# Kernel tuning notes

Hardware: AMD Instinct MI355X
Metric: run time of the kernel (lower is better)

Reference implementation:

```python
import jax, jax.numpy as jnp
import numpy as np

SPATIAL_SHAPES = [(116, 200), (58, 100), (29, 50), (15, 25)]  # (H, W) per level
NUM_HEADS = 8
NUM_LEVELS = 4
NUM_POINTS = 8
NUM_Z = 4  # num_Z_anchors; NUM_POINTS must be divisible by NUM_Z
EMBED = 256


def _msda3d_forward(query, value, reference_points, w_off, b_off, w_attn, b_attn, w_val, b_val):
    bs, nq, _ = query.shape
    d = EMBED // NUM_HEADS
    # value projection -> (bs, num_value, heads, d)
    v = (value @ w_val + b_val).reshape(bs, -1, NUM_HEADS, d)
    # sampling offsets and attention weights from query
    off = (query @ w_off + b_off).reshape(bs, nq, NUM_HEADS, NUM_LEVELS, NUM_POINTS, 2)
    attn = (query @ w_attn + b_attn).reshape(bs, nq, NUM_HEADS, NUM_LEVELS * NUM_POINTS)
    attn = jax.nn.softmax(attn, axis=-1).reshape(bs, nq, NUM_HEADS, NUM_LEVELS, NUM_POINTS)
    # normalize offsets by (W, H) per level
    shapes = jnp.asarray(SPATIAL_SHAPES, dtype=query.dtype)  # (L,2) = (h,w)
    norm = jnp.stack([shapes[:, 1], shapes[:, 0]], axis=-1)  # (L,2) = (w,h)
    off = off / norm[None, None, None, :, None, :]
    # reference_points (bs,nq,Z,2) broadcast against offsets split over Z anchors
    p_per_z = NUM_POINTS // NUM_Z
    off = off.reshape(bs, nq, NUM_HEADS, NUM_LEVELS, p_per_z, NUM_Z, 2)
    loc = reference_points[:, :, None, None, None, :, :] + off
    loc = loc.reshape(bs, nq, NUM_HEADS, NUM_LEVELS, NUM_POINTS, 2)
    # per-level bilinear sampling (grid_sample, align_corners=False, zeros padding)
    out = jnp.zeros((bs, nq, NUM_HEADS, d), dtype=query.dtype)
    start = 0
    for lvl, (H, W) in enumerate(SPATIAL_SHAPES):
        v_l = v[:, start:start + H * W]  # (bs, H*W, heads, d)
        start += H * W
        locs = loc[:, :, :, lvl]  # (bs, nq, heads, P, 2) in [0,1]
        # grid = 2*loc-1, then unnormalize with align_corners=False: x = loc*W - 0.5
        x = locs[..., 0] * W - 0.5
        y = locs[..., 1] * H - 0.5
        x0 = jnp.floor(x)
        y0 = jnp.floor(y)
        lx = x - x0
        ly = y - y0
        x0i = x0.astype(jnp.int32)
        y0i = y0.astype(jnp.int32)
        samp = jnp.zeros((bs, nq, NUM_HEADS, NUM_POINTS, d), dtype=query.dtype)
        corners = ((0, 0, (1 - ly) * (1 - lx)), (0, 1, (1 - ly) * lx),
                   (1, 0, ly * (1 - lx)), (1, 1, ly * lx))
        for dy, dx, w in corners:
            xi = x0i + dx
            yi = y0i + dy
            valid = (xi >= 0) & (xi < W) & (yi >= 0) & (yi < H)
            idx = jnp.clip(yi, 0, H - 1) * W + jnp.clip(xi, 0, W - 1)  # (bs,nq,heads,P)
            # gather along flattened HW per (batch, head)
            idx2 = idx.transpose(0, 1, 3, 2).reshape(bs, nq * NUM_POINTS, NUM_HEADS)
            g = jnp.take_along_axis(v_l, idx2[..., None], axis=1)  # (bs, nq*P, heads, d)
            g = g.reshape(bs, nq, NUM_POINTS, NUM_HEADS, d).transpose(0, 1, 3, 2, 4)
            samp = samp + g * (w * valid.astype(query.dtype))[..., None]
        out = out + (samp * attn[:, :, :, lvl, :, None]).sum(axis=3)
    return out.reshape(bs, nq, EMBED)


def setup_inputs() -> dict:
    key = jax.random.key(0)
    ks = jax.random.split(key, 9)
    bs, nq = 6, 10000
    num_value = sum(h * w for h, w in SPATIAL_SHAPES)  # 30825
    return {
        "query": jax.random.normal(ks[0], (bs, nq, EMBED), jnp.float32),
        "value": jax.random.normal(ks[1], (bs, num_value, EMBED), jnp.float32),
        "reference_points": jax.random.uniform(ks[2], (bs, nq, NUM_Z, 2), jnp.float32),
        "w_off": jax.random.normal(ks[3], (EMBED, NUM_HEADS * NUM_LEVELS * NUM_POINTS * 2), jnp.float32) * 0.01,
        "b_off": jax.random.normal(ks[4], (NUM_HEADS * NUM_LEVELS * NUM_POINTS * 2,), jnp.float32) * 0.02,
        "w_attn": jax.random.normal(ks[5], (EMBED, NUM_HEADS * NUM_LEVELS * NUM_POINTS), jnp.float32) * 0.02,
        "b_attn": jnp.zeros((NUM_HEADS * NUM_LEVELS * NUM_POINTS,), jnp.float32),
        "w_val": jax.random.normal(ks[6], (EMBED, EMBED), jnp.float32) * 0.02,
        "b_val": jnp.zeros((EMBED,), jnp.float32),
    }


def reference(query, value, reference_points, w_off, b_off, w_attn, b_attn, w_val, b_val):
    return _msda3d_forward(query, value, reference_points, w_off, b_off, w_attn, b_attn, w_val, b_val)
```

## Files before the change

kernel.cpp:

```cpp
#include <hip/hip_runtime.h>
#include <hip/hip_bf16.h>

#define NQ 10000
#define BS 6
#define NV 30825

typedef __attribute__((ext_vector_type(8))) short bf16x8;
typedef __attribute__((ext_vector_type(8))) unsigned short u16x8;
typedef __attribute__((ext_vector_type(4))) float f32x4;
typedef __attribute__((ext_vector_type(2))) float f32x2;

__device__ __forceinline__ void gload_lds16(const void* g, void* l) {
  __builtin_amdgcn_global_load_lds(
      (const __attribute__((address_space(1))) unsigned int*)g,
      (__attribute__((address_space(3))) unsigned int*)l, 16, 0, 0);
}

__device__ __forceinline__ unsigned short bf_bits(float f) {
  __hip_bfloat16 h = __float2bfloat16(f);
  return *(unsigned short*)&h;
}

__global__ __launch_bounds__(256) void prep_weights_kernel(
    const float* __restrict__ w_val, const float* __restrict__ w_off,
    const float* __restrict__ w_attn, const float* __restrict__ b_off,
    const float* __restrict__ b_attn, unsigned short* __restrict__ wvalT,
    unsigned short* __restrict__ wpackT, float* __restrict__ bpack) {
  int i = blockIdx.x * 256 + threadIdx.x;
  if (i < 65536) {
    int n = i >> 8, k = i & 255;
    wvalT[i] = bf_bits(w_val[k * 256 + n]);
  } else if (i < 65536 + 196608) {
    int j = i - 65536;
    int n = j >> 8, k = j & 255;
    float v = (n < 512) ? w_off[k * 512 + n] : w_attn[k * 256 + (n - 512)];
    wpackT[j] = bf_bits(v);
  } else if (i < 65536 + 196608 + 768) {
    int j = i - 262144;
    bpack[j] = (j < 512) ? b_off[j] : b_attn[j - 512];
  }
}

__global__ __launch_bounds__(256) void gemm_mfma_kernel(
    const float* __restrict__ A, const unsigned short* __restrict__ WT,
    const float* __restrict__ bias, unsigned short* __restrict__ C, int M, int N) {
  __shared__ short As[128 * 64];
  __shared__ short Bs[128 * 64];
  const int tid = threadIdx.x;
  const int wv = tid >> 6;
  const int lane = tid & 63;
  const int wr = wv >> 1, wc = wv & 1;
  const int m0 = blockIdx.x * 128;
  const int n0 = blockIdx.y * 128;

  f32x4 acc[4][4] = {};

  for (int kt = 0; kt < 4; ++kt) {
#pragma unroll
    for (int j = 0; j < 4; ++j) {
      int u = j * 256 + tid;
      int row = u >> 3;
      int kbyte = (u & 7) * 16;
      int ldsoff = (j * 256 + wv * 64) * 16;
      gload_lds16((const char*)WT + (size_t)(n0 + row) * 512 + kt * 128 + kbyte,
                  (char*)Bs + ldsoff);
    }
#pragma unroll
    for (int j = 0; j < 4; ++j) {
      int u = j * 256 + tid;
      int row = u >> 3, oct = u & 7;
      int gr = m0 + row; if (gr >= M) gr = M - 1;
      const float4* ap = (const float4*)(A + (size_t)gr * 256 + kt * 64 + oct * 8);
      float4 a0 = ap[0], a1 = ap[1];
      u16x8 pk = { bf_bits(a0.x), bf_bits(a0.y), bf_bits(a0.z), bf_bits(a0.w),
                   bf_bits(a1.x), bf_bits(a1.y), bf_bits(a1.z), bf_bits(a1.w) };
      *(u16x8*)&As[row * 64 + oct * 8] = pk;
    }
    __syncthreads();
#pragma unroll
    for (int kk = 0; kk < 2; ++kk) {
      bf16x8 af[4], bfr[4];
#pragma unroll
      for (int mi = 0; mi < 4; ++mi) {
        int off = (wr * 64 + mi * 16 + (lane & 15)) * 64 + kk * 32 + (lane >> 4) * 8;
        af[mi] = *(const bf16x8*)&As[off];
      }
#pragma unroll
      for (int ni = 0; ni < 4; ++ni) {
        int off = (wc * 64 + ni * 16 + (lane & 15)) * 64 + kk * 32 + (lane >> 4) * 8;
        bfr[ni] = *(const bf16x8*)&Bs[off];
      }
#pragma unroll
      for (int mi = 0; mi < 4; ++mi)
#pragma unroll
        for (int ni = 0; ni < 4; ++ni)
          acc[mi][ni] = __builtin_amdgcn_mfma_f32_16x16x32_bf16(
              af[mi], bfr[ni], acc[mi][ni], 0, 0, 0);
    }
    __syncthreads();
  }

  const int colb = n0 + wc * 64 + (lane & 15);
  float bvn[4];
#pragma unroll
  for (int ni = 0; ni < 4; ++ni) bvn[ni] = bias[colb + ni * 16];
#pragma unroll
  for (int mi = 0; mi < 4; ++mi) {
#pragma unroll
    for (int r = 0; r < 4; ++r) {
      int row = m0 + wr * 64 + mi * 16 + (lane >> 4) * 4 + r;
      if (row < M) {
#pragma unroll
        for (int ni = 0; ni < 4; ++ni)
          C[(size_t)row * N + colb + ni * 16] = bf_bits(acc[mi][ni][r] + bvn[ni]);
      }
    }
  }
}

__global__ __launch_bounds__(256) void msda_sample_kernel(
    const __hip_bfloat16* __restrict__ vproj,
    const __hip_bfloat16* __restrict__ C2,
    const float* __restrict__ ref,
    float* __restrict__ out) {
  const int bq = blockIdx.x;
  const int b = bq / NQ;
  const int tid = threadIdx.x;

  __shared__ int   s_idx[4][256];
  __shared__ float s_w[4][256];

  {
    const int lp = tid & 31;
    const int l = lp >> 3, p = lp & 7, z = p & 3;
    const __hip_bfloat162* offp = (const __hip_bfloat162*)(C2 + (size_t)bq * 768);
    __hip_bfloat162 ob = offp[tid];
    float ox = __bfloat162float(ob.x), oy = __bfloat162float(ob.y);
    float logit = __bfloat162float(C2[(size_t)bq * 768 + 512 + tid]);

    float mx = logit;
#pragma unroll
    for (int m = 16; m >= 1; m >>= 1) mx = fmaxf(mx, __shfl_xor(mx, m, 32));
    float e = __expf(logit - mx);
    float s = e;
#pragma unroll
    for (int m = 16; m >= 1; m >>= 1) s += __shfl_xor(s, m, 32);
    float aw = e / s;

    float2 rz = *(const float2*)(ref + (size_t)bq * 8 + z * 2);
    const int W = 200 >> l;
    const int H = (l == 3) ? 15 : (116 >> l);
    const int base = (l == 0) ? 0 : (l == 1) ? 23200 : (l == 2) ? 29000 : 30450;

    float x = rz.x * (float)W + ox - 0.5f;
    float y = rz.y * (float)H + oy - 0.5f;
    float x0f = floorf(x), y0f = floorf(y);
    float lx = x - x0f, ly = y - y0f;
    int x0 = (int)x0f, y0 = (int)y0f;
    int x1 = x0 + 1, y1 = y0 + 1;

    float w00 = (1.f - ly) * (1.f - lx) * aw;
    float w01 = (1.f - ly) * lx * aw;
    float w10 = ly * (1.f - lx) * aw;
    float w11 = ly * lx * aw;

    if (!((x0 >= 0) & (x0 < W))) { w00 = 0.f; w10 = 0.f; }
    if (!((x1 >= 0) & (x1 < W))) { w01 = 0.f; w11 = 0.f; }
    if (!((y0 >= 0) & (y0 < H))) { w00 = 0.f; w01 = 0.f; }
    if (!((y1 >= 0) & (y1 < H))) { w10 = 0.f; w11 = 0.f; }

    int x0c = min(max(x0, 0), W - 1);
    int x1c = min(max(x1, 0), W - 1);
    int y0c = min(max(y0, 0), H - 1);
    int y1c = min(max(y1, 0), H - 1);

    s_idx[0][tid] = base + y0c * W + x0c;  s_w[0][tid] = w00;
    s_idx[1][tid] = base + y0c * W + x1c;  s_w[1][tid] = w01;
    s_idx[2][tid] = base + y1c * W + x0c;  s_w[2][tid] = w10;
    s_idx[3][tid] = base + y1c * W + x1c;  s_w[3][tid] = w11;
  }
  __syncthreads();

  const int h = tid >> 5;
  const int lane32 = tid & 31;
  const int e = lane32 & 3;
  const int sibase = tid & ~3;
  const char* vrow = (const char*)vproj + (size_t)b * NV * 512 + h * 64 + e * 16;

  f32x2 acc0 = {0.f, 0.f}, acc1 = {0.f, 0.f}, acc2 = {0.f, 0.f}, acc3 = {0.f, 0.f};
#pragma unroll
  for (int s = 0; s < 4; ++s) {
    const int si = sibase + s;
#pragma unroll
    for (int c = 0; c < 4; ++c) {
      int row = s_idx[c][si];
      float w = s_w[c][si];
      uint4 v = *(const uint4*)(vrow + (row << 9));
      f32x2 wv = {w, w};
      f32x2 p0 = {__uint_as_float(v.x << 16), __uint_as_float(v.x & 0xffff0000u)};
      f32x2 p1 = {__uint_as_float(v.y << 16), __uint_as_float(v.y & 0xffff0000u)};
      f32x2 p2 = {__uint_as_float(v.z << 16), __uint_as_float(v.z & 0xffff0000u)};
      f32x2 p3 = {__uint_as_float(v.w << 16), __uint_as_float(v.w & 0xffff0000u)};
      acc0 += wv * p0;
      acc1 += wv * p1;
      acc2 += wv * p2;
      acc3 += wv * p3;
    }
  }

#pragma unroll
  for (int m = 4; m <= 16; m <<= 1) {
    acc0.x += __shfl_xor(acc0.x, m, 32);  acc0.y += __shfl_xor(acc0.y, m, 32);
    acc1.x += __shfl_xor(acc1.x, m, 32);  acc1.y += __shfl_xor(acc1.y, m, 32);
    acc2.x += __shfl_xor(acc2.x, m, 32);  acc2.y += __shfl_xor(acc2.y, m, 32);
    acc3.x += __shfl_xor(acc3.x, m, 32);  acc3.y += __shfl_xor(acc3.y, m, 32);
  }

  if (lane32 < 4) {
    float4* op = (float4*)(out + (size_t)bq * 256 + h * 32 + e * 8);
    op[0] = make_float4(acc0.x, acc0.y, acc1.x, acc1.y);
    op[1] = make_float4(acc2.x, acc2.y, acc3.x, acc3.y);
  }
}

extern "C" void kernel_launch(void* const* d_in, const int* in_sizes, int n_in,
                              void* d_out, int out_size, void* d_ws, size_t ws_size,
                              hipStream_t stream) {
  const float* query  = (const float*)d_in[0];
  const float* value  = (const float*)d_in[1];
  const float* refp   = (const float*)d_in[2];
  const float* w_off  = (const float*)d_in[3];
  const float* b_off  = (const float*)d_in[4];
  const float* w_attn = (const float*)d_in[5];
  const float* b_attn = (const float*)d_in[6];
  const float* w_val  = (const float*)d_in[7];
  const float* b_val  = (const float*)d_in[8];
  float* out = (float*)d_out;

  char* ws = (char*)d_ws;
  unsigned short* vproj  = (unsigned short*)(ws);
  unsigned short* C2     = (unsigned short*)(ws + 94694400);
  unsigned short* wvalT  = (unsigned short*)(ws + 186854400);
  unsigned short* wpackT = (unsigned short*)(ws + 186985472);
  float*          bpack  = (float*)        (ws + 187378688);

  const int Mv = BS * NV;
  const int Mq = BS * NQ;

  prep_weights_kernel<<<1032, 256, 0, stream>>>(w_val, w_off, w_attn, b_off, b_attn,
                                                wvalT, wpackT, bpack);
  gemm_mfma_kernel<<<dim3((Mv + 127) / 128, 2), 256, 0, stream>>>(
      value, wvalT, b_val, vproj, Mv, 256);
  gemm_mfma_kernel<<<dim3((Mq + 127) / 128, 6), 256, 0, stream>>>(
      query, wpackT, bpack, C2, Mq, 768);
  msda_sample_kernel<<<BS * NQ, 256, 0, stream>>>(
      (const __hip_bfloat16*)vproj, (const __hip_bfloat16*)C2, refp, out);
}
```

Measured before the change: 452.7 us.

## Scatter value projection into per-head row layout and fetch two x-neighbors per load

The value GEMM epilogue now writes its output in a per-level layout of (y, head, x, 32 channels), so the two horizontally adjacent corners of a head's bilinear sample sit in one contiguous 128-byte span. The sampler merges the x0/x1 corners into a single pixel pair, clamping the left x to W-2 and remapping the weights. Each corner-pair is then fetched by 8 lanes with one 16-byte load each, replacing four separate corner loads per point. This aims to cut scattered gather transactions in the sampling kernel. The price is uncoalesced scattered stores and integer divisions in the GEMM epilogue.

```diff
diff --git a/kernel.cpp b/kernel.cpp
--- a/kernel.cpp
+++ b/kernel.cpp
@@ -4,6 +4,7 @@
 #define NQ 10000
 #define BS 6
 #define NV 30825
+
 
 typedef __attribute__((ext_vector_type(8))) short bf16x8;
 typedef __attribute__((ext_vector_type(8))) unsigned short u16x8;
@@ -41,6 +42,7 @@
   }
 }
 
+template <bool SCATTER>
 __global__ __launch_bounds__(256) void gemm_mfma_kernel(
     const float* __restrict__ A, const unsigned short* __restrict__ WT,
     const float* __restrict__ bias, unsigned short* __restrict__ C, int M, int N) {
@@ -109,10 +111,26 @@
 #pragma unroll
     for (int r = 0; r < 4; ++r) {
       int row = m0 + wr * 64 + mi * 16 + (lane >> 4) * 4 + r;
-      if (row < M) {
+      if (row >= M) continue;
+      if (!SCATTER) {
 #pragma unroll
         for (int ni = 0; ni < 4; ++ni)
           C[(size_t)row * N + colb + ni * 16] = bf_bits(acc[mi][ni][r] + bvn[ni]);
+      } else {
+        int b = row / NV;
+        int pix = row - b * NV;
+        int ubase, Wl, y, x;
+        if (pix < 23200)      { int pl = pix;         y = pl / 200; x = pl - y * 200; ubase = 0;      Wl = 200; }
+        else if (pix < 29000) { int pl = pix - 23200; y = pl / 100; x = pl - y * 100; ubase = 185600; Wl = 100; }
+        else if (pix < 30450) { int pl = pix - 29000; y = pl / 50;  x = pl - y * 50;  ubase = 232000; Wl = 50;  }
+        else                  { int pl = pix - 30450; y = pl / 25;  x = pl - y * 25;  ubase = 243600; Wl = 25;  }
+        size_t bu = (size_t)b * 246600 + ubase + (size_t)(y * 8) * Wl + x;
+#pragma unroll
+        for (int ni = 0; ni < 4; ++ni) {
+          int col = colb + ni * 16;
+          int h = col >> 5, ch = col & 31;
+          C[(bu + (size_t)h * Wl) * 32 + ch] = bf_bits(acc[mi][ni][r] + bvn[ni]);
+        }
       }
     }
   }
@@ -127,10 +145,11 @@
   const int b = bq / NQ;
   const int tid = threadIdx.x;
 
-  __shared__ int   s_idx[4][256];
-  __shared__ float s_w[4][256];
+  __shared__ int    s_pidx[512];
+  __shared__ float2 s_w2[512];
 
   {
+    const int h = tid >> 5;
     const int lp = tid & 31;
     const int l = lp >> 3, p = lp & 7, z = p & 3;
     const __hip_bfloat162* offp = (const __hip_bfloat162*)(C2 + (size_t)bq * 768);
@@ -148,9 +167,9 @@
     float aw = e / s;
 
     float2 rz = *(const float2*)(ref + (size_t)bq * 8 + z * 2);
-    const int W = 200 >> l;
-    const int H = (l == 3) ? 15 : (116 >> l);
-    const int base = (l == 0) ? 0 : (l == 1) ? 23200 : (l == 2) ? 29000 : 30450;
+    const int W = (l == 0) ? 200 : (l == 1) ? 100 : (l == 2) ? 50 : 25;
+    const int H = (l == 0) ? 116 : (l == 1) ? 58 : (l == 2) ? 29 : 15;
+    const int ub = (l == 0) ? 0 : (l == 1) ? 185600 : (l == 2) ? 232000 : 243600;
 
     float x = rz.x * (float)W + ox - 0.5f;
     float y = rz.y * (float)H + oy - 0.5f;
@@ -159,53 +178,52 @@
     int x0 = (int)x0f, y0 = (int)y0f;
     int x1 = x0 + 1, y1 = y0 + 1;
 
-    float w00 = (1.f - ly) * (1.f - lx) * aw;
-    float w01 = (1.f - ly) * lx * aw;
-    float w10 = ly * (1.f - lx) * aw;
-    float w11 = ly * lx * aw;
-
-    if (!((x0 >= 0) & (x0 < W))) { w00 = 0.f; w10 = 0.f; }
-    if (!((x1 >= 0) & (x1 < W))) { w01 = 0.f; w11 = 0.f; }
-    if (!((y0 >= 0) & (y0 < H))) { w00 = 0.f; w01 = 0.f; }
-    if (!((y1 >= 0) & (y1 < H))) { w10 = 0.f; w11 = 0.f; }
-
+    float wx0 = 1.f - lx, wx1 = lx;
+    if (!((x0 >= 0) & (x0 < W))) wx0 = 0.f;
+    if (!((x1 >= 0) & (x1 < W))) wx1 = 0.f;
+    float wy0 = (1.f - ly) * aw, wy1 = ly * aw;
+    if (!((y0 >= 0) & (y0 < H))) wy0 = 0.f;
+    if (!((y1 >= 0) & (y1 < H))) wy1 = 0.f;
+
+    int px  = min(max(x0, 0), W - 2);
     int x0c = min(max(x0, 0), W - 1);
     int x1c = min(max(x1, 0), W - 1);
+    float wA = (x0c == px     ? wx0 : 0.f) + (x1c == px     ? wx1 : 0.f);
+    float wB = (x0c == px + 1 ? wx0 : 0.f) + (x1c == px + 1 ? wx1 : 0.f);
     int y0c = min(max(y0, 0), H - 1);
     int y1c = min(max(y1, 0), H - 1);
 
-    s_idx[0][tid] = base + y0c * W + x0c;  s_w[0][tid] = w00;
-    s_idx[1][tid] = base + y0c * W + x1c;  s_w[1][tid] = w01;
-    s_idx[2][tid] = base + y1c * W + x0c;  s_w[2][tid] = w10;
-    s_idx[3][tid] = base + y1c * W + x1c;  s_w[3][tid] = w11;
+    const int g = h * 4 + l;
+    const int t0 = (p * 2 + 0) * 32 + g;
+    s_pidx[t0]      = ub + (y0c * 8 + h) * W + px;
+    s_w2[t0]        = make_float2(wy0 * wA, wy0 * wB);
+    s_pidx[t0 + 32] = ub + (y1c * 8 + h) * W + px;
+    s_w2[t0 + 32]   = make_float2(wy1 * wA, wy1 * wB);
   }
   __syncthreads();
 
-  const int h = tid >> 5;
-  const int lane32 = tid & 31;
-  const int e = lane32 & 3;
-  const int sibase = tid & ~3;
-  const char* vrow = (const char*)vproj + (size_t)b * NV * 512 + h * 64 + e * 16;
+  const int g = tid >> 3;
+  const int lane8 = tid & 7;
+  const int colhalf = lane8 >> 2;
+  const char* vbb = (const char*)vproj + (size_t)b * 15782400 + lane8 * 16;
 
   f32x2 acc0 = {0.f, 0.f}, acc1 = {0.f, 0.f}, acc2 = {0.f, 0.f}, acc3 = {0.f, 0.f};
 #pragma unroll
-  for (int s = 0; s < 4; ++s) {
-    const int si = sibase + s;
-#pragma unroll
-    for (int c = 0; c < 4; ++c) {
-      int row = s_idx[c][si];
-      float w = s_w[c][si];
-      uint4 v = *(const uint4*)(vrow + (row << 9));
-      f32x2 wv = {w, w};
-      f32x2 p0 = {__uint_as_float(v.x << 16), __uint_as_float(v.x & 0xffff0000u)};
-      f32x2 p1 = {__uint_as_float(v.y << 16), __uint_as_float(v.y & 0xffff0000u)};
-      f32x2 p2 = {__uint_as_float(v.z << 16), __uint_as_float(v.z & 0xffff0000u)};
-      f32x2 p3 = {__uint_as_float(v.w << 16), __uint_as_float(v.w & 0xffff0000u)};
-      acc0 += wv * p0;
-      acc1 += wv * p1;
-      acc2 += wv * p2;
-      acc3 += wv * p3;
-    }
+  for (int t = 0; t < 16; ++t) {
+    int idx = t * 32 + g;
+    int pidx = s_pidx[idx];
+    float2 w2 = s_w2[idx];
+    float w = colhalf ? w2.y : w2.x;
+    uint4 v = *(const uint4*)(vbb + ((size_t)(unsigned)pidx << 6));
+    f32x2 wv = {w, w};
+    f32x2 p0 = {__uint_as_float(v.x << 16), __uint_as_float(v.x & 0xffff0000u)};
+    f32x2 p1 = {__uint_as_float(v.y << 16), __uint_as_float(v.y & 0xffff0000u)};
+    f32x2 p2 = {__uint_as_float(v.z << 16), __uint_as_float(v.z & 0xffff0000u)};
+    f32x2 p3 = {__uint_as_float(v.w << 16), __uint_as_float(v.w & 0xffff0000u)};
+    acc0 += wv * p0;
+    acc1 += wv * p1;
+    acc2 += wv * p2;
+    acc3 += wv * p3;
   }
 
 #pragma unroll
@@ -216,7 +234,9 @@
     acc3.x += __shfl_xor(acc3.x, m, 32);  acc3.y += __shfl_xor(acc3.y, m, 32);
   }
 
-  if (lane32 < 4) {
+  if ((tid & 31) < 4) {
+    const int h = tid >> 5;
+    const int e = tid & 3;
     float4* op = (float4*)(out + (size_t)bq * 256 + h * 32 + e * 8);
     op[0] = make_float4(acc0.x, acc0.y, acc1.x, acc1.y);
     op[1] = make_float4(acc2.x, acc2.y, acc3.x, acc3.y);
@@ -249,9 +269,9 @@
 
   prep_weights_kernel<<<1032, 256, 0, stream>>>(w_val, w_off, w_attn, b_off, b_attn,
                                                 wvalT, wpackT, bpack);
-  gemm_mfma_kernel<<<dim3((Mv + 127) / 128, 2), 256, 0, stream>>>(
+  gemm_mfma_kernel<true><<<dim3((Mv + 127) / 128, 2), 256, 0, stream>>>(
       value, wvalT, b_val, vproj, Mv, 256);
-  gemm_mfma_kernel<<<dim3((Mq + 127) / 128, 6), 256, 0, stream>>>(
+  gemm_mfma_kernel<false><<<dim3((Mq + 127) / 128, 6), 256, 0, stream>>>(
       query, wpackT, bpack, C2, Mq, 768);
   msda_sample_kernel<<<BS * NQ, 256, 0, stream>>>(
       (const __hip_bfloat16*)vproj, (const __hip_bfloat16*)C2, refp, out);
```

Measured after the change: 468.7 us. 3.5% more time.
